# Kernel optimization log

Measured on AMD Instinct MI355X. Metric: run time of the kernel, lower is better.

Reference implementation:

```python
import jax, jax.numpy as jnp
import numpy as np

BS, DEG, H = 32, 4, 32
OUT = H  # n_aggr=1 inside Full -> out_size = n_aggr * h_size = h_size


def setup_inputs() -> dict:
    key = jax.random.key(0)
    k1, k2 = jax.random.split(key)
    neighbour_h = jax.random.normal(k1, (BS, DEG, H), dtype=jnp.float32)
    hp1 = H + 1
    t_shape = (hp1,) * DEG + (OUT,)  # [33,33,33,33,32]
    # xavier_uniform-like scale: fan_in = hp1**DEG, fan_out = OUT
    scale = float(np.sqrt(2.0 / (hp1 ** DEG + OUT)))
    T = jax.random.normal(k2, t_shape, dtype=jnp.float32) * scale
    return {"neighbour_h": neighbour_h, "T": T}


def reference(neighbour_h, T):
    # Full.forward: chunk neighbour_h along child dim, feed to AugmentedTensor.
    # AugmentedTensor: sequentially contract T against each child's augmented
    # embedding [h_i ; 1] over the leading axes of T.
    bs, deg, h = neighbour_h.shape
    hp1 = h + 1
    # augment with trailing 1 (bias slot): [bs, deg, h+1]
    h_aug = jnp.concatenate(
        [neighbour_h, jnp.ones((bs, deg, 1), neighbour_h.dtype)], axis=2
    )
    # first contraction: [bs, hp1] @ [hp1, hp1^(deg-1)*out]
    res = jnp.matmul(h_aug[:, 0, :], T.reshape(hp1, -1))
    # remaining contractions shrink the trailing dim by hp1 each step
    for i in range(1, deg):
        res = jnp.einsum("bi,bio->bo", h_aug[:, i, :], res.reshape(bs, hp1, -1))
    return res  # [bs, out_size] == [bs, h_size] since n_aggr=1
```

## Files before the change

### kernel.cpp

```cpp
#include <hip/hip_runtime.h>

#define HSZ 32
#define HP1 33
#define M3 35937
#define M3P 35952
#define TI_STRIDE 1149984
#define NBLK 2247
#define NT 64

#define OFF_A0T   0
#define OFF_D     8192
#define OFF_TILES 4610048

typedef short bf16x8 __attribute__((ext_vector_type(8)));
typedef float f32x16 __attribute__((ext_vector_type(16)));

__device__ inline short f2bf(float f) {
  unsigned u = __builtin_bit_cast(unsigned, f);
  u += 0x7FFFu + ((u >> 16) & 1u);
  return (short)(u >> 16);
}

__global__ __launch_bounds__(256) void k_pre(const float* __restrict__ nh,
                                             float* __restrict__ a0T,
                                             float* __restrict__ D,
                                             float* __restrict__ tiles) {
  const int b = blockIdx.y;
  const int m = blockIdx.x * 256 + threadIdx.x;
  if (m < M3P) {
    float v = 0.f;
    if (m < M3) {
      const int j = m / 1089;
      const int r = m - j * 1089;
      const int k = r / 33;
      const int l = r - k * 33;
      const float a1 = (j < HSZ) ? nh[(b * 4 + 1) * HSZ + j] : 1.0f;
      const float a2 = (k < HSZ) ? nh[(b * 4 + 2) * HSZ + k] : 1.0f;
      const float a3 = (l < HSZ) ? nh[(b * 4 + 3) * HSZ + l] : 1.0f;
      v = a1 * a2 * a3;
    }
    D[(size_t)b * M3P + m] = v;
  }
  if (blockIdx.x == 0 && threadIdx.x < HP1) {
    const int i = threadIdx.x;
    a0T[i * 32 + b] = (i < HSZ) ? nh[(b * 4 + 0) * HSZ + i] : 1.0f;
  }
  if (b == 1 && blockIdx.x < 64) {
    ((float4*)tiles)[blockIdx.x * 256 + threadIdx.x] =
        make_float4(0.f, 0.f, 0.f, 0.f);
  }
}

__global__ __launch_bounds__(64) void k_main(const float* __restrict__ T,
                                             const float* __restrict__ a0T,
                                             const float* __restrict__ D,
                                             float* __restrict__ tiles) {
  const int blk = blockIdx.x;
  const int m0 = blk * 16;
  const int l = (int)threadIdx.x;
  const int bo = l & 31;
  const int g = l >> 5;

  const float* dp = D + (size_t)bo * M3P + m0 + 8 * g;
  float df[8];
  *(float4*)(df)     = *(const float4*)(dp);
  *(float4*)(df + 4) = *(const float4*)(dp + 4);

  size_t toff[8];
#pragma unroll
  for (int e = 0; e < 8; ++e) {
    int mm = m0 + 8 * g + e;
    if (mm > M3 - 1) mm = M3 - 1;
    toff[e] = (size_t)mm * 32 + bo;
  }

  f32x16 acc = {};

  float tv[8];
#pragma unroll
  for (int e = 0; e < 8; ++e) tv[e] = T[toff[e]];
  float a0c = a0T[bo];

  for (int i = 0; i < HP1; ++i) {
    float tn[8];
    float a0n = 0.f;
    if (i < HP1 - 1) {
      const float* Tn = T + (size_t)(i + 1) * TI_STRIDE;
#pragma unroll
      for (int e = 0; e < 8; ++e) tn[e] = Tn[toff[e]];
      a0n = a0T[(i + 1) * 32 + bo];
    }
    bf16x8 af, bfr;
#pragma unroll
    for (int e = 0; e < 8; ++e) {
      af[e]  = f2bf(a0c * df[e]);
      bfr[e] = f2bf(tv[e]);
    }
    acc = __builtin_amdgcn_mfma_f32_32x32x16_bf16(af, bfr, acc, 0, 0, 0);
#pragma unroll
    for (int e = 0; e < 8; ++e) tv[e] = tn[e];
    a0c = a0n;
  }

  float* tp = tiles + (size_t)(blk & (NT - 1)) * 1024;
#pragma unroll
  for (int r = 0; r < 16; ++r) {
    const int brow = (r & 3) + 8 * (r >> 2) + 4 * g;
    atomicAdd(tp + brow * 32 + bo, acc[r]);
  }
}

__global__ __launch_bounds__(256) void k_red(const float* __restrict__ tiles,
                                             float* __restrict__ out) {
  const int idx = blockIdx.x * 256 + (int)threadIdx.x;
  float s = 0.f;
  for (int t = 0; t < NT; ++t) s += tiles[(size_t)t * 1024 + idx];
  out[idx] = s;
}

extern "C" void kernel_launch(void* const* d_in, const int* in_sizes, int n_in,
                              void* d_out, int out_size, void* d_ws, size_t ws_size,
                              hipStream_t stream) {
  const float* nh = (const float*)d_in[0];
  const float* T  = (const float*)d_in[1];
  float* out = (float*)d_out;
  char* ws = (char*)d_ws;
  float* a0T   = (float*)(ws + OFF_A0T);
  float* D     = (float*)(ws + OFF_D);
  float* tiles = (float*)(ws + OFF_TILES);

  k_pre<<<dim3(141, 32), 256, 0, stream>>>(nh, a0T, D, tiles);
  k_main<<<NBLK, 64, 0, stream>>>(T, a0T, D, tiles);
  k_red<<<4, 256, 0, stream>>>(tiles, out);
}
```

Baseline: 43.35 us.

## Fuse precompute into main kernel, deepen T prefetch, replace atomics with per-block tiles

```diff
diff --git a/kernel.cpp b/kernel.cpp
--- a/kernel.cpp
+++ b/kernel.cpp
@@ -3,14 +3,9 @@
 #define HSZ 32
 #define HP1 33
 #define M3 35937
-#define M3P 35952
 #define TI_STRIDE 1149984
-#define NBLK 2247
-#define NT 64
-
-#define OFF_A0T   0
-#define OFF_D     8192
-#define OFF_TILES 4610048
+#define NBLK 1124
+#define NCH 2
 
 typedef short bf16x8 __attribute__((ext_vector_type(8)));
 typedef float f32x16 __attribute__((ext_vector_type(16)));
@@ -21,101 +16,97 @@
   return (short)(u >> 16);
 }
 
-__global__ __launch_bounds__(256) void k_pre(const float* __restrict__ nh,
-                                             float* __restrict__ a0T,
-                                             float* __restrict__ D,
+__global__ __launch_bounds__(64) void k_main(const float* __restrict__ T,
+                                             const float* __restrict__ nh,
                                              float* __restrict__ tiles) {
-  const int b = blockIdx.y;
-  const int m = blockIdx.x * 256 + threadIdx.x;
-  if (m < M3P) {
-    float v = 0.f;
-    if (m < M3) {
-      const int j = m / 1089;
-      const int r = m - j * 1089;
-      const int k = r / 33;
-      const int l = r - k * 33;
-      const float a1 = (j < HSZ) ? nh[(b * 4 + 1) * HSZ + j] : 1.0f;
-      const float a2 = (k < HSZ) ? nh[(b * 4 + 2) * HSZ + k] : 1.0f;
-      const float a3 = (l < HSZ) ? nh[(b * 4 + 3) * HSZ + l] : 1.0f;
-      v = a1 * a2 * a3;
-    }
-    D[(size_t)b * M3P + m] = v;
-  }
-  if (blockIdx.x == 0 && threadIdx.x < HP1) {
-    const int i = threadIdx.x;
-    a0T[i * 32 + b] = (i < HSZ) ? nh[(b * 4 + 0) * HSZ + i] : 1.0f;
-  }
-  if (b == 1 && blockIdx.x < 64) {
-    ((float4*)tiles)[blockIdx.x * 256 + threadIdx.x] =
-        make_float4(0.f, 0.f, 0.f, 0.f);
-  }
-}
-
-__global__ __launch_bounds__(64) void k_main(const float* __restrict__ T,
-                                             const float* __restrict__ a0T,
-                                             const float* __restrict__ D,
-                                             float* __restrict__ tiles) {
-  const int blk = blockIdx.x;
-  const int m0 = blk * 16;
   const int l = (int)threadIdx.x;
   const int bo = l & 31;
   const int g = l >> 5;
+  f32x16 acc = {};
 
-  const float* dp = D + (size_t)bo * M3P + m0 + 8 * g;
-  float df[8];
-  *(float4*)(df)     = *(const float4*)(dp);
-  *(float4*)(df + 4) = *(const float4*)(dp + 4);
+  for (int c = 0; c < NCH; ++c) {
+    const int m0 = ((int)blockIdx.x * NCH + c) * 16;
 
-  size_t toff[8];
+    float df[8];
+    int ioff[8];
 #pragma unroll
-  for (int e = 0; e < 8; ++e) {
-    int mm = m0 + 8 * g + e;
-    if (mm > M3 - 1) mm = M3 - 1;
-    toff[e] = (size_t)mm * 32 + bo;
+    for (int e = 0; e < 8; ++e) {
+      const int mm = m0 + 8 * g + e;
+      const bool valid = mm < M3;
+      const int mc = valid ? mm : (M3 - 1);
+      const int j = mc / 1089;
+      const int r = mc - j * 1089;
+      const int kk = r / 33;
+      const int ll = r - kk * 33;
+      const float a1 = (j < HSZ) ? nh[(bo * 4 + 1) * HSZ + j] : 1.0f;
+      const float a2 = (kk < HSZ) ? nh[(bo * 4 + 2) * HSZ + kk] : 1.0f;
+      const float a3 = (ll < HSZ) ? nh[(bo * 4 + 3) * HSZ + ll] : 1.0f;
+      df[e] = valid ? (a1 * a2 * a3) : 0.0f;
+      ioff[e] = mc * 32 + bo;
+    }
+
+#define LOADT(buf, row)                                   \
+  {                                                       \
+    const float* Tp = T + (size_t)(row) * TI_STRIDE;      \
+    _Pragma("unroll")                                     \
+    for (int e = 0; e < 8; ++e) buf[e] = Tp[ioff[e]];     \
+  }
+#define COMP(buf, a0v)                                                     \
+  {                                                                        \
+    bf16x8 af, bfr;                                                        \
+    _Pragma("unroll")                                                      \
+    for (int e = 0; e < 8; ++e) {                                          \
+      af[e] = f2bf((a0v) * df[e]);                                         \
+      bfr[e] = f2bf(buf[e]);                                               \
+    }                                                                      \
+    acc = __builtin_amdgcn_mfma_f32_32x32x16_bf16(af, bfr, acc, 0, 0, 0);  \
   }
 
-  f32x16 acc = {};
-
-  float tv[8];
-#pragma unroll
-  for (int e = 0; e < 8; ++e) tv[e] = T[toff[e]];
-  float a0c = a0T[bo];
-
-  for (int i = 0; i < HP1; ++i) {
-    float tn[8];
-    float a0n = 0.f;
-    if (i < HP1 - 1) {
-      const float* Tn = T + (size_t)(i + 1) * TI_STRIDE;
-#pragma unroll
-      for (int e = 0; e < 8; ++e) tn[e] = Tn[toff[e]];
-      a0n = a0T[(i + 1) * 32 + bo];
+    float tA[8], tB[8], tC[8];
+    float aA, aB, aC;
+    LOADT(tA, 0);
+    aA = nh[bo * 128 + 0];
+    LOADT(tB, 1);
+    aB = nh[bo * 128 + 1];
+    for (int i = 0; i < 30; i += 3) {
+      LOADT(tC, i + 2);
+      aC = nh[bo * 128 + i + 2];
+      COMP(tA, aA);
+      LOADT(tA, i + 3);
+      aA = nh[bo * 128 + i + 3];
+      COMP(tB, aB);
+      LOADT(tB, i + 4);
+      aB = nh[bo * 128 + i + 4];
+      COMP(tC, aC);
     }
-    bf16x8 af, bfr;
-#pragma unroll
-    for (int e = 0; e < 8; ++e) {
-      af[e]  = f2bf(a0c * df[e]);
-      bfr[e] = f2bf(tv[e]);
-    }
-    acc = __builtin_amdgcn_mfma_f32_32x32x16_bf16(af, bfr, acc, 0, 0, 0);
-#pragma unroll
-    for (int e = 0; e < 8; ++e) tv[e] = tn[e];
-    a0c = a0n;
+    LOADT(tC, 32);
+    aC = 1.0f;
+    COMP(tA, aA);
+    COMP(tB, aB);
+    COMP(tC, aC);
+#undef LOADT
+#undef COMP
   }
 
-  float* tp = tiles + (size_t)(blk & (NT - 1)) * 1024;
+  float* tp = tiles + (size_t)blockIdx.x * 1024;
 #pragma unroll
   for (int r = 0; r < 16; ++r) {
     const int brow = (r & 3) + 8 * (r >> 2) + 4 * g;
-    atomicAdd(tp + brow * 32 + bo, acc[r]);
+    tp[brow * 32 + bo] = acc[r];
   }
 }
 
 __global__ __launch_bounds__(256) void k_red(const float* __restrict__ tiles,
                                              float* __restrict__ out) {
   const int idx = blockIdx.x * 256 + (int)threadIdx.x;
-  float s = 0.f;
-  for (int t = 0; t < NT; ++t) s += tiles[(size_t)t * 1024 + idx];
-  out[idx] = s;
+  float s0 = 0.f, s1 = 0.f, s2 = 0.f, s3 = 0.f;
+  for (int t = 0; t < NBLK; t += 4) {
+    s0 += tiles[(size_t)(t + 0) * 1024 + idx];
+    s1 += tiles[(size_t)(t + 1) * 1024 + idx];
+    s2 += tiles[(size_t)(t + 2) * 1024 + idx];
+    s3 += tiles[(size_t)(t + 3) * 1024 + idx];
+  }
+  out[idx] = (s0 + s1) + (s2 + s3);
 }
 
 extern "C" void kernel_launch(void* const* d_in, const int* in_sizes, int n_in,
@@ -124,12 +115,8 @@
   const float* nh = (const float*)d_in[0];
   const float* T  = (const float*)d_in[1];
   float* out = (float*)d_out;
-  char* ws = (char*)d_ws;
-  float* a0T   = (float*)(ws + OFF_A0T);
-  float* D     = (float*)(ws + OFF_D);
-  float* tiles = (float*)(ws + OFF_TILES);
+  float* tiles = (float*)d_ws;
 
-  k_pre<<<dim3(141, 32), 256, 0, stream>>>(nh, a0T, D, tiles);
-  k_main<<<NBLK, 64, 0, stream>>>(T, a0T, D, tiles);
+  k_main<<<NBLK, 64, 0, stream>>>(T, nh, tiles);
   k_red<<<4, 256, 0, stream>>>(tiles, out);
 }
```

Result: slower. 68.03 us (+56.9%).
